# Kernel tuning notes

Hardware: AMD Instinct MI355X
Metric: run time of the kernel (lower is better)

Reference implementation:

```python
import jax, jax.numpy as jnp
import numpy as np

NEG_INF = -1e30  # stand-in for float('-inf') that is softmax-safe


def setup_inputs() -> dict:
    key = jax.random.key(0)
    ks = jax.random.split(key, 6)
    B, H, S, D = 2, 8, 1024, 64
    NF, K = 4, 3
    return {
        "query": jax.random.normal(ks[0], (B, H, S, D), dtype=jnp.float32),
        "keys": jax.random.normal(ks[1], (B, H, S, D), dtype=jnp.float32),
        "vals": jax.random.normal(ks[2], (B, H, S, D), dtype=jnp.float32),
        "mask": jnp.ones((B, 1, S, S), dtype=jnp.int32),
        "conv_w": jax.random.normal(ks[3], (NF, 1, K, K), dtype=jnp.float32) * (1.0 / K),
        "conv_b": jnp.zeros((NF,), dtype=jnp.float32),
        "lin_w": jax.random.normal(ks[4], (1, NF), dtype=jnp.float32) * 0.5,
        "lin_b": jnp.zeros((1,), dtype=jnp.float32),
    }


def reference(query, keys, vals, mask, conv_w, conv_b, lin_w, lin_b):
    B, H, S, D = query.shape
    NF = conv_w.shape[0]
    K = conv_w.shape[2]
    scale = jnp.asarray(D, query.dtype) ** 0.5

    # [B,H,S,S] raw dot-product scores
    dp = jnp.einsum("bhsd,bhtd->bhst", query, keys) / scale

    # conv2d over the score matrix: treat (B*H) as batch, 1 input channel
    x = dp.reshape(B * H, 1, S, S)
    conv = jax.lax.conv_general_dilated(
        x, conv_w,
        window_strides=(1, 1),
        padding=[(K // 2, K // 2), (K // 2, K // 2)],
        dimension_numbers=("NCHW", "OIHW", "NCHW"),
    ) + conv_b[None, :, None, None]
    conv = jax.nn.leaky_relu(conv, negative_slope=0.01)  # [B*H, NF, S, S]

    # per-pixel linear over the filter axis (Linear(num_filters, 1))
    conv = conv.reshape(B, H, NF, S, S)
    preattn = jnp.einsum("bhfst,f->bhst", conv, lin_w[0]) + lin_b[0]

    # masking + softmax (mask broadcasts over heads)
    preattn = jnp.where(mask == 0, jnp.asarray(NEG_INF, preattn.dtype), preattn)
    attn = jax.nn.softmax(preattn, axis=-1)

    # dropout is identity in eval mode
    return jnp.einsum("bhst,bhtd->bhsd", attn, vals)
```

## Files before the change

### kernel.cpp

```cpp
#include <hip/hip_runtime.h>
#include <math.h>

#define S_LEN 1024
#define D_DIM 64
#define NBH   16
#define RPB   14
#define NSB   74

typedef unsigned short ushort_t;
typedef unsigned int uint_t;
typedef __attribute__((ext_vector_type(8))) _Float16 half8;
typedef __attribute__((ext_vector_type(2))) _Float16 h2;
typedef __attribute__((ext_vector_type(4))) short short4v;
typedef __attribute__((ext_vector_type(4))) float f32x4;

__device__ __forceinline__ ushort_t f16bits(float x) {
    _Float16 h = (_Float16)x;
    ushort_t b;
    __builtin_memcpy(&b, &h, 2);
    return b;
}
__device__ __forceinline__ float uniform_f(float x) {
    return __int_as_float(__builtin_amdgcn_readfirstlane(__float_as_int(x)));
}
__device__ __forceinline__ float fast_exp2(float x) {
#if __has_builtin(__builtin_amdgcn_exp2f)
    return __builtin_amdgcn_exp2f(x);
#else
    return exp2f(x);
#endif
}
__device__ __forceinline__ half8 ld_half8_b64(const ushort_t* p) {
    union { uint2 u[2]; half8 h; } c;
    c.u[0] = *(const uint2*)p;
    c.u[1] = *(const uint2*)(p + 4);
    return c.h;
}

__global__ __launch_bounds__(256) void prep(
    const float* __restrict__ k, const float* __restrict__ v,
    const int* __restrict__ mask, const float* __restrict__ conv_w,
    ushort_t* __restrict__ kh, ushort_t* __restrict__ vh,
    unsigned* __restrict__ mw, ushort_t* __restrict__ wtab)
{
    __shared__ float Ls[64][65];
    const int tid = threadIdx.x;
    const int bx = blockIdx.x;
    if (bx < 512) {
        const int gid  = bx * 256 + tid;
        const int bh   = gid >> 13;
        const int tile = (gid >> 7) & 63;
        const int ch   = (gid >> 6) & 1;
        const int lane = gid & 63;
        const int quad = lane >> 4, t15 = lane & 15;
        const float* src = k + ((size_t)bh * S_LEN + tile * 16 + t15) * D_DIM
                             + ch * 32 + quad * 8;
        float x[8];
        *(float4*)(x + 0) = *(const float4*)(src);
        *(float4*)(x + 4) = *(const float4*)(src + 4);
        ushort_t hv[8];
        #pragma unroll
        for (int i = 0; i < 8; ++i) hv[i] = f16bits(x[i] * 0.125f);
        *(short4v*)(kh + (size_t)gid * 8)     = *(short4v*)(hv);
        *(short4v*)(kh + (size_t)gid * 8 + 4) = *(short4v*)(hv + 4);
    } else if (bx < 768) {
        const int bi = bx - 512;
        const int tt = bi & 15, bh = bi >> 4;
        const float* vb = v + ((size_t)bh * S_LEN + tt * 64) * D_DIM;
        #pragma unroll
        for (int p = 0; p < 4; ++p) {
            int idx = p * 1024 + tid * 4;
            int r = idx >> 6, c = idx & 63;
            float4 x = *(const float4*)(vb + r * 64 + c);
            Ls[r][c] = x.x; Ls[r][c+1] = x.y; Ls[r][c+2] = x.z; Ls[r][c+3] = x.w;
        }
        __syncthreads();
        const int d = tid >> 2, c0 = (tid & 3) * 16;
        ushort_t hi[16];
        #pragma unroll
        for (int j = 0; j < 16; ++j) hi[j] = f16bits(Ls[c0 + j][d]);
        const int tb0 = tt * 8 + (c0 >> 3);
        const size_t o0 = (((size_t)bh * 128 + tb0) * 64 + d) * 8;
        const size_t o1 = (((size_t)bh * 128 + tb0 + 1) * 64 + d) * 8;
        *(short4v*)(vh + o0)     = *(short4v*)(hi);
        *(short4v*)(vh + o0 + 4) = *(short4v*)(hi + 4);
        *(short4v*)(vh + o1)     = *(short4v*)(hi + 8);
        *(short4v*)(vh + o1 + 4) = *(short4v*)(hi + 12);
    } else if (bx < 1024) {
        const int gid = (bx - 768) * 256 + tid;
        const int row = gid >> 5, wd = gid & 31;
        const int4* mp = (const int4*)(mask + (size_t)row * 1024 + wd * 32);
        unsigned bits = 0;
        #pragma unroll
        for (int p = 0; p < 8; ++p) {
            int4 qv = mp[p];
            bits |= (qv.x != 0 ? 1u : 0u) << (p * 4 + 0);
            bits |= (qv.y != 0 ? 1u : 0u) << (p * 4 + 1);
            bits |= (qv.z != 0 ? 1u : 0u) << (p * 4 + 2);
            bits |= (qv.w != 0 ? 1u : 0u) << (p * 4 + 3);
        }
        mw[(size_t)row * 32 + wd] = bits;
    } else {
        if (tid < 64) {
            const int o = tid & 15, qd = tid >> 4;
            half8* wt = (half8*)wtab;
            #pragma unroll
            for (int f = 0; f < 4; ++f) {
                half8 fr0 = {}, fr1 = {}, fr2 = {};
                #pragma unroll
                for (int i = 0; i < 8; ++i) {
                    const int kk = qd * 8 + i;
                    const int r  = kk & 15;
                    const bool hiK = kk < 16;
                    #pragma unroll
                    for (int dr = 0; dr < 3; ++dr) {
                        if (r - o == dr - 1) {
                            const float w0 = conv_w[f*9 + dr*3 + 0];
                            const float w1 = conv_w[f*9 + dr*3 + 1];
                            const float w2 = conv_w[f*9 + dr*3 + 2];
                            const _Float16 w0h = (_Float16)w0;
                            const _Float16 w1h = (_Float16)w1;
                            const _Float16 w2h = (_Float16)w2;
                            const _Float16 w0l = (_Float16)(w0 - (float)w0h);
                            const _Float16 w1l = (_Float16)(w1 - (float)w1h);
                            const _Float16 w2l = (_Float16)(w2 - (float)w2h);
                            fr0[i] = hiK ? w0h : w1h;
                            fr1[i] = hiK ? w0l : w1l;
                            fr2[i] = hiK ? w2h : w2l;
                        }
                    }
                }
                wt[(f*3 + 0) * 64 + tid] = fr0;
                wt[(f*3 + 1) * 64 + tid] = fr1;
                wt[(f*3 + 2) * 64 + tid] = fr2;
            }
        }
    }
}

#define DPTSTR 20
#define PSTR   1048
__global__ __launch_bounds__(512) void fused_qk_conv_av(
    const float* __restrict__ q,
    const ushort_t* __restrict__ kh, const unsigned* __restrict__ mw,
    const ushort_t* __restrict__ vh, const ushort_t* __restrict__ wtab,
    const float* __restrict__ conv_b,
    const float* __restrict__ lin_w, const float* __restrict__ lin_b,
    float* __restrict__ out)
{
    __shared__ ushort_t sBuf[1028 * DPTSTR];
    __shared__ float oBuf[16][68];
    __shared__ float lsRow[16];
    __shared__ unsigned mbT[32][16];

    const int st = blockIdx.x, bh = blockIdx.y;
    const int s0 = st * RPB;
    const int b  = bh >> 3;
    const int tid = threadIdx.x;
    const int wave = tid >> 6, lane = tid & 63;
    const int m = lane & 15, quad = lane >> 4;

    half8 WF[4][3];
    {
        const half8* wt = (const half8*)wtab;
        #pragma unroll
        for (int f = 0; f < 4; ++f)
            #pragma unroll
            for (int g = 0; g < 3; ++g)
                WF[f][g] = wt[(f*3 + g) * 64 + lane];
    }

    {
        const int wd = tid >> 4, o = tid & 15;
        const int s = s0 - 1 + o;
        mbT[wd][o] = (s >= 0 && s < S_LEN)
                   ? mw[((size_t)b * S_LEN + s) * 32 + wd] : 0u;
    }
    if (tid < 32) {
        const int row = (tid < 16) ? 1 : 1026;
        sBuf[row * DPTSTR + (tid & 15)] = 0;
    }

    const int sA = s0 - 1 + m;
    const int sQ = sA < 0 ? 0 : (sA > S_LEN - 1 ? S_LEN - 1 : sA);
    const float* qp = q + ((size_t)bh * S_LEN + sQ) * D_DIM + quad * 8;
    float qa[16];
    *(float4*)(qa + 0)  = *(const float4*)(qp + 0);
    *(float4*)(qa + 4)  = *(const float4*)(qp + 4);
    *(float4*)(qa + 8)  = *(const float4*)(qp + 32);
    *(float4*)(qa + 12) = *(const float4*)(qp + 36);
    half8 AH0, AH1;
    #pragma unroll
    for (int i = 0; i < 8; ++i) {
        AH0[i] = (_Float16)qa[i];
        AH1[i] = (_Float16)qa[8 + i];
    }

    #pragma unroll
    for (int tt = 0; tt < 8; ++tt) {
        const int tile = wave * 8 + tt;
        const size_t kb = (((size_t)bh * 64 + tile) * 128 + lane) * 8;
        half8 KH0 = *(const half8*)(kh + kb);
        half8 KH1 = *(const half8*)(kh + kb + 512);
        f32x4 a = {0.f, 0.f, 0.f, 0.f};
        a = __builtin_amdgcn_mfma_f32_16x16x32_f16(AH0, KH0, a, 0, 0, 0);
        a = __builtin_amdgcn_mfma_f32_16x16x32_f16(AH1, KH1, a, 0, 0, 0);
        ushort_t t4[4];
        #pragma unroll
        for (int r = 0; r < 4; ++r) {
            const int s = s0 - 1 + quad * 4 + r;
            const float v = (s >= 0 && s < S_LEN) ? a[r] : 0.f;
            t4[r] = f16bits(v);
        }
        uint2 wv2;
        wv2.x = (uint_t)t4[0] | ((uint_t)t4[1] << 16);
        wv2.y = (uint_t)t4[2] | ((uint_t)t4[3] << 16);
        *(uint2*)&sBuf[(tile * 16 + m + 2) * DPTSTR + quad * 4] = wv2;
    }

    const float L2E = 1.44269504088896341f;
    float cb[4], aF[4], bF[4];
    #pragma unroll
    for (int f = 0; f < 4; ++f) {
        cb[f] = conv_b[f];
        const float lwf = lin_w[f];
        aF[f] = uniform_f(0.505f * lwf * L2E);
        bF[f] = uniform_f(0.495f * lwf * L2E);
    }
    const float lbE = uniform_f(lin_b[0] * L2E);

    __syncthreads();

    const int i01 = (m + 1 + (quad >> 1)) * DPTSTR + (quad & 1) * 8
                  + wave * (8 * 16 * DPTSTR);
    const int i22 = (m + 3) * DPTSTR + (quad & 1) * 8
                  + wave * (8 * 16 * DPTSTR);
    uint_t Ps[16];
    #pragma unroll
    for (int tt = 0; tt < 8; ++tt) {
        const int tile = wave * 8 + tt;
        half8 B01 = ld_half8_b64(&sBuf[i01 + tt * (16 * DPTSTR)]);
        half8 B22 = ld_half8_b64(&sBuf[i22 + tt * (16 * DPTSTR)]);
        f32x4 acc[4];
        #pragma unroll
        for (int f = 0; f < 4; ++f) {
            const float cbf = cb[f];
            acc[f] = (f32x4){cbf, cbf, cbf, cbf};
            acc[f] = __builtin_amdgcn_mfma_f32_16x16x32_f16(WF[f][0], B01, acc[f], 0, 0, 0);
            acc[f] = __builtin_amdgcn_mfma_f32_16x16x32_f16(WF[f][1], B01, acc[f], 0, 0, 0);
            acc[f] = __builtin_amdgcn_mfma_f32_16x16x32_f16(WF[f][2], B22, acc[f], 0, 0, 0);
        }
        const uint4 mq = *(const uint4*)&mbT[tile >> 1][quad * 4];
        const int cbit = ((tile & 1) << 4) + m;
        float pv[4];
        #pragma unroll
        for (int r = 0; r < 4; ++r) {
            const int o = quad * 4 + r;
            const bool act = (o >= 1) && (o <= RPB) && (s0 - 1 + o < S_LEN);
            float pre = lbE;
            #pragma unroll
            for (int f = 0; f < 4; ++f) {
                const float y = acc[f][r];
                pre = fmaf(aF[f], y, pre);
                pre = fmaf(bF[f], fabsf(y), pre);
            }
            const unsigned mword = (r == 0) ? mq.x : (r == 1) ? mq.y
                                 : (r == 2) ? mq.z : mq.w;
            const bool keep = act && ((mword >> cbit) & 1u);
            pv[r] = fast_exp2(keep ? pre : -1e30f);
        }
        Ps[2*tt + 0] = (uint_t)f16bits(pv[0]) | ((uint_t)f16bits(pv[1]) << 16);
        Ps[2*tt + 1] = (uint_t)f16bits(pv[2]) | ((uint_t)f16bits(pv[3]) << 16);
    }
    __syncthreads();

    #pragma unroll
    for (int tt = 0; tt < 8; ++tt) {
        const int c = (wave * 8 + tt) * 16 + m;
        ushort_t* pp = &sBuf[quad * 4 * PSTR + c];
        const uint_t lo = Ps[2*tt], hi = Ps[2*tt + 1];
        pp[0]        = (ushort_t)lo;
        pp[PSTR]     = (ushort_t)(lo >> 16);
        pp[2*PSTR]   = (ushort_t)hi;
        pp[3*PSTR]   = (ushort_t)(hi >> 16);
    }
    __syncthreads();

    const int d0 = (wave & 3) * 16;
    const int th = wave >> 2;
    f32x4 O  = {0.f, 0.f, 0.f, 0.f};
    f32x4 RS = {0.f, 0.f, 0.f, 0.f};
    half8 ONE;
    #pragma unroll
    for (int i = 0; i < 8; ++i) ONE[i] = (_Float16)1.0f;
    const ushort_t* ph_base = &sBuf[m * PSTR + th * 512 + quad * 8];
    const ushort_t* vv_base = vh + ((size_t)bh * 65536
                                    + (size_t)(th * 64 + quad) * 512
                                    + (size_t)(d0 + m) * 8);
    #pragma unroll 4
    for (int i = 0; i < 16; ++i) {
        half8 ph = *(const half8*)(ph_base + i * 32);
        half8 vv = *(const half8*)(vv_base + (size_t)i * 2048);
        O  = __builtin_amdgcn_mfma_f32_16x16x32_f16(ph, vv, O, 0, 0, 0);
        RS = __builtin_amdgcn_mfma_f32_16x16x32_f16(ph, ONE, RS, 0, 0, 0);
    }
    if (wave < 4) {
        #pragma unroll
        for (int r = 0; r < 4; ++r) oBuf[quad * 4 + r][d0 + m] = O[r];
    }
    if (wave == 0 && m == 0) {
        #pragma unroll
        for (int r = 0; r < 4; ++r) lsRow[quad * 4 + r] = RS[r];
    }
    __syncthreads();
    if (wave >= 4) {
        #pragma unroll
        for (int r = 0; r < 4; ++r) {
            const int br = quad * 4 + r;
            const int s = s0 - 1 + br;
            if (br >= 1 && br <= RPB && s < S_LEN) {
                const float lsum = lsRow[br] + RS[r];
                out[((size_t)bh * S_LEN + s) * D_DIM + d0 + m] =
                    (O[r] + oBuf[br][d0 + m]) / lsum;
            }
        }
    }
}

extern "C" void kernel_launch(void* const* d_in, const int* in_sizes, int n_in,
                              void* d_out, int out_size, void* d_ws, size_t ws_size,
                              hipStream_t stream) {
    const float* q      = (const float*)d_in[0];
    const float* k      = (const float*)d_in[1];
    const float* v      = (const float*)d_in[2];
    const int*   mask   = (const int*)d_in[3];
    const float* conv_w = (const float*)d_in[4];
    const float* conv_b = (const float*)d_in[5];
    const float* lin_w  = (const float*)d_in[6];
    const float* lin_b  = (const float*)d_in[7];
    float* out = (float*)d_out;

    char* wsb = (char*)d_ws;
    const size_t MB = 1024 * 1024;
    ushort_t* kh   = (ushort_t*)(wsb + 0 * MB);
    ushort_t* vh   = (ushort_t*)(wsb + 2 * MB);
    unsigned* mw   = (unsigned*)(wsb + 4 * MB);
    ushort_t* wtab = (ushort_t*)(wsb + 4 * MB + 256 * 1024);

    prep<<<dim3(1025), 256, 0, stream>>>(k, v, mask, conv_w, kh, vh, mw, wtab);
    fused_qk_conv_av<<<dim3(NSB, NBH), 512, 0, stream>>>(
        q, kh, mw, vh, wtab, conv_b, lin_w, lin_b, out);
}
```

Before: 130.5 us.

## Swizzle score LDS layout, stream conv weights per filter, raise occupancy

Replaces the padded-stride score buffer (stride 20) with a dense 16-wide layout using an XOR-like rotation swizzle to avoid bank conflicts while shrinking LDS. Conv weight fragments and per-filter coefficients are no longer held in registers for the whole kernel; they are reloaded inside a non-unrolled filter loop that processes two tiles at once. Launch bounds now request 8 waves per SIMD-level occupancy, trading extra global/L1 weight loads for fewer VGPRs and smaller LDS footprint. The PSTR for the P buffer is also reduced, which must still fit within the smaller sBuf.

```diff
diff --git a/kernel.cpp b/kernel.cpp
--- a/kernel.cpp
+++ b/kernel.cpp
@@ -30,11 +30,13 @@
     return exp2f(x);
 #endif
 }
-__device__ __forceinline__ half8 ld_half8_b64(const ushort_t* p) {
-    union { uint2 u[2]; half8 h; } c;
-    c.u[0] = *(const uint2*)p;
-    c.u[1] = *(const uint2*)(p + 4);
+__device__ __forceinline__ half8 mk8(uint2 a, uint2 b) {
+    union { uint_t u[4]; half8 h; } c;
+    c.u[0] = a.x; c.u[1] = a.y; c.u[2] = b.x; c.u[3] = b.y;
     return c.h;
+}
+__device__ __forceinline__ int swz(int row, int unit) {
+    return (row << 4) + (((unit + (row >> 2)) & 3) << 2);
 }
 
 __global__ __launch_bounds__(256) void prep(
@@ -138,9 +140,8 @@
     }
 }
 
-#define DPTSTR 20
-#define PSTR   1048
-__global__ __launch_bounds__(512) void fused_qk_conv_av(
+#define PSTR 1032
+__global__ __launch_bounds__(512, 8) void fused_qk_conv_av(
     const float* __restrict__ q,
     const ushort_t* __restrict__ kh, const unsigned* __restrict__ mw,
     const ushort_t* __restrict__ vh, const ushort_t* __restrict__ wtab,
@@ -148,7 +149,7 @@
     const float* __restrict__ lin_w, const float* __restrict__ lin_b,
     float* __restrict__ out)
 {
-    __shared__ ushort_t sBuf[1028 * DPTSTR];
+    __shared__ ushort_t sBuf[16512];
     __shared__ float oBuf[16][68];
     __shared__ float lsRow[16];
     __shared__ unsigned mbT[32][16];
@@ -160,16 +161,6 @@
     const int wave = tid >> 6, lane = tid & 63;
     const int m = lane & 15, quad = lane >> 4;
 
-    half8 WF[4][3];
-    {
-        const half8* wt = (const half8*)wtab;
-        #pragma unroll
-        for (int f = 0; f < 4; ++f)
-            #pragma unroll
-            for (int g = 0; g < 3; ++g)
-                WF[f][g] = wt[(f*3 + g) * 64 + lane];
-    }
-
     {
         const int wd = tid >> 4, o = tid & 15;
         const int s = s0 - 1 + o;
@@ -178,7 +169,7 @@
     }
     if (tid < 32) {
         const int row = (tid < 16) ? 1 : 1026;
-        sBuf[row * DPTSTR + (tid & 15)] = 0;
+        sBuf[(row << 4) + (tid & 15)] = 0;
     }
 
     const int sA = s0 - 1 + m;
@@ -215,62 +206,76 @@
         uint2 wv2;
         wv2.x = (uint_t)t4[0] | ((uint_t)t4[1] << 16);
         wv2.y = (uint_t)t4[2] | ((uint_t)t4[3] << 16);
-        *(uint2*)&sBuf[(tile * 16 + m + 2) * DPTSTR + quad * 4] = wv2;
+        *(uint2*)&sBuf[swz(tile * 16 + m + 2, quad)] = wv2;
     }
 
     const float L2E = 1.44269504088896341f;
-    float cb[4], aF[4], bF[4];
-    #pragma unroll
-    for (int f = 0; f < 4; ++f) {
-        cb[f] = conv_b[f];
-        const float lwf = lin_w[f];
-        aF[f] = uniform_f(0.505f * lwf * L2E);
-        bF[f] = uniform_f(0.495f * lwf * L2E);
-    }
     const float lbE = uniform_f(lin_b[0] * L2E);
 
     __syncthreads();
 
-    const int i01 = (m + 1 + (quad >> 1)) * DPTSTR + (quad & 1) * 8
-                  + wave * (8 * 16 * DPTSTR);
-    const int i22 = (m + 3) * DPTSTR + (quad & 1) * 8
-                  + wave * (8 * 16 * DPTSTR);
+    const int u0 = (quad & 1) << 1;
+    const int rB = m + 1 + (quad >> 1);
     uint_t Ps[16];
     #pragma unroll
-    for (int tt = 0; tt < 8; ++tt) {
-        const int tile = wave * 8 + tt;
-        half8 B01 = ld_half8_b64(&sBuf[i01 + tt * (16 * DPTSTR)]);
-        half8 B22 = ld_half8_b64(&sBuf[i22 + tt * (16 * DPTSTR)]);
-        f32x4 acc[4];
-        #pragma unroll
+    for (int p = 0; p < 4; ++p) {
+        const int tileA = wave * 8 + p * 2;
+        const int baseA = tileA * 16;
+        half8 BA01 = mk8(*(const uint2*)&sBuf[swz(baseA + rB, u0)],
+                         *(const uint2*)&sBuf[swz(baseA + rB, u0 + 1)]);
+        half8 BA22 = mk8(*(const uint2*)&sBuf[swz(baseA + m + 3, u0)],
+                         *(const uint2*)&sBuf[swz(baseA + m + 3, u0 + 1)]);
+        half8 BB01 = mk8(*(const uint2*)&sBuf[swz(baseA + 16 + rB, u0)],
+                         *(const uint2*)&sBuf[swz(baseA + 16 + rB, u0 + 1)]);
+        half8 BB22 = mk8(*(const uint2*)&sBuf[swz(baseA + 16 + m + 3, u0)],
+                         *(const uint2*)&sBuf[swz(baseA + 16 + m + 3, u0 + 1)]);
+        float preA[4], preB[4];
+        #pragma unroll
+        for (int r = 0; r < 4; ++r) { preA[r] = lbE; preB[r] = lbE; }
+        #pragma unroll 1
         for (int f = 0; f < 4; ++f) {
-            const float cbf = cb[f];
-            acc[f] = (f32x4){cbf, cbf, cbf, cbf};
-            acc[f] = __builtin_amdgcn_mfma_f32_16x16x32_f16(WF[f][0], B01, acc[f], 0, 0, 0);
-            acc[f] = __builtin_amdgcn_mfma_f32_16x16x32_f16(WF[f][1], B01, acc[f], 0, 0, 0);
-            acc[f] = __builtin_amdgcn_mfma_f32_16x16x32_f16(WF[f][2], B22, acc[f], 0, 0, 0);
-        }
-        const uint4 mq = *(const uint4*)&mbT[tile >> 1][quad * 4];
-        const int cbit = ((tile & 1) << 4) + m;
-        float pv[4];
+            const half8* wp = (const half8*)wtab + f * 192 + lane;
+            const half8 W0 = wp[0];
+            const half8 W1 = wp[64];
+            const half8 W2 = wp[128];
+            const float cbf = conv_b[f];
+            const float lwf = lin_w[f];
+            const float af  = uniform_f(0.505f * lwf * L2E);
+            const float bf2 = uniform_f(0.495f * lwf * L2E);
+            f32x4 aA = {cbf, cbf, cbf, cbf};
+            f32x4 aB = {cbf, cbf, cbf, cbf};
+            aA = __builtin_amdgcn_mfma_f32_16x16x32_f16(W0, BA01, aA, 0, 0, 0);
+            aB = __builtin_amdgcn_mfma_f32_16x16x32_f16(W0, BB01, aB, 0, 0, 0);
+            aA = __builtin_amdgcn_mfma_f32_16x16x32_f16(W1, BA01, aA, 0, 0, 0);
+            aB = __builtin_amdgcn_mfma_f32_16x16x32_f16(W1, BB01, aB, 0, 0, 0);
+            aA = __builtin_amdgcn_mfma_f32_16x16x32_f16(W2, BA22, aA, 0, 0, 0);
+            aB = __builtin_amdgcn_mfma_f32_16x16x32_f16(W2, BB22, aB, 0, 0, 0);
+            #pragma unroll
+            for (int r = 0; r < 4; ++r) {
+                const float yA = aA[r], yB = aB[r];
+                preA[r] = fmaf(af, yA, preA[r]);
+                preA[r] = fmaf(bf2, fabsf(yA), preA[r]);
+                preB[r] = fmaf(af, yB, preB[r]);
+                preB[r] = fmaf(bf2, fabsf(yB), preB[r]);
+            }
+        }
+        const uint4 mq = *(const uint4*)&mbT[(tileA >> 1)][quad * 4];
+        float pvA[4], pvB[4];
         #pragma unroll
         for (int r = 0; r < 4; ++r) {
             const int o = quad * 4 + r;
             const bool act = (o >= 1) && (o <= RPB) && (s0 - 1 + o < S_LEN);
-            float pre = lbE;
-            #pragma unroll
-            for (int f = 0; f < 4; ++f) {
-                const float y = acc[f][r];
-                pre = fmaf(aF[f], y, pre);
-                pre = fmaf(bF[f], fabsf(y), pre);
-            }
             const unsigned mword = (r == 0) ? mq.x : (r == 1) ? mq.y
                                  : (r == 2) ? mq.z : mq.w;
-            const bool keep = act && ((mword >> cbit) & 1u);
-            pv[r] = fast_exp2(keep ? pre : -1e30f);
-        }
-        Ps[2*tt + 0] = (uint_t)f16bits(pv[0]) | ((uint_t)f16bits(pv[1]) << 16);
-        Ps[2*tt + 1] = (uint_t)f16bits(pv[2]) | ((uint_t)f16bits(pv[3]) << 16);
+            const bool kA = act && ((mword >> m) & 1u);
+            const bool kB = act && ((mword >> (16 + m)) & 1u);
+            pvA[r] = fast_exp2(kA ? preA[r] : -1e30f);
+            pvB[r] = fast_exp2(kB ? preB[r] : -1e30f);
+        }
+        Ps[p*4 + 0] = (uint_t)f16bits(pvA[0]) | ((uint_t)f16bits(pvA[1]) << 16);
+        Ps[p*4 + 1] = (uint_t)f16bits(pvA[2]) | ((uint_t)f16bits(pvA[3]) << 16);
+        Ps[p*4 + 2] = (uint_t)f16bits(pvB[0]) | ((uint_t)f16bits(pvB[1]) << 16);
+        Ps[p*4 + 3] = (uint_t)f16bits(pvB[2]) | ((uint_t)f16bits(pvB[3]) << 16);
     }
     __syncthreads();
 
```

Result: slower. 144.6 us (+10.8%).
